# Kernel optimization log

Hardware: AMD Instinct MI355X
Metric: run time of the kernel (lower is better)

## Reference

```python
import jax, jax.numpy as jnp
import numpy as np

B, N, ZDIM = 8, 2048, 128
NPOINTS = 32
BN_EPS = 1e-5


def setup_inputs() -> dict:
    key = jax.random.key(0)
    ks = iter(jax.random.split(key, 64))

    def w(shape, s=0.05):
        return jax.random.normal(next(ks), shape, jnp.float32) * s

    inp = {"x": jax.random.normal(next(ks), (B, N, 3), jnp.float32)}
    inp.update(dict(
        w1=w((128, 3)), b1=w((128,)),
        w2=w((128, 128)), b2=w((128,)),
        w3=w((256, 128)), b3=w((256,)),
        w4=w((512, 256)), b4=w((512,)),
        a1_wqk=w((32, 1)), a1_wt=w((128, 128)), a1_bt=w((128,)),
        a2_wqk=w((32, 1)), a2_wt=w((128, 128)), a2_bt=w((128,)),
        a3_wqk=w((64, 1)), a3_wt=w((256, 256)), a3_bt=w((256,)),
        a4_wqk=w((128, 1)), a4_wt=w((512, 512)), a4_bt=w((512,)),
        fc1m_w=w((256, 512)), fc1m_b=w((256,)),
        fc2m_w=w((128, 256)), fc2m_b=w((128,)),
        fc3m_w=w((ZDIM, 128)), fc3m_b=w((ZDIM,)),
        fc1v_w=w((256, 512)), fc1v_b=w((256,)),
        fc2v_w=w((128, 256)), fc2v_b=w((128,)),
        fc3v_w=w((1, 128)), fc3v_b=w((1,)),
    ))
    return inp


def bn_cn(h):
    # BatchNorm1d over [B, C, N] features (training-mode batch stats, affine=identity at init)
    m = h.mean(axis=(0, 2), keepdims=True)
    v = h.var(axis=(0, 2), keepdims=True)
    return (h - m) * jax.lax.rsqrt(v + BN_EPS)


def bn_f(h):
    # BatchNorm1d over [B, F]
    m = h.mean(axis=0, keepdims=True)
    v = h.var(axis=0, keepdims=True)
    return (h - m) * jax.lax.rsqrt(v + BN_EPS)


def conv1x1(h, w, b):
    # 1x1 Conv1d: [B,Cin,N] x [Cout,Cin] -> [B,Cout,N]
    return jnp.einsum('oc,bcn->bon', w, h) + b[None, :, None]


def angle_density(xyz):
    # xyz: [B,N,3]; 1 - cosine similarity between all point pairs (computed as GEMM,
    # never materializing the [B,N,N,3] expanded tensors of the torch code)
    xn = xyz / jnp.linalg.norm(xyz, axis=-1, keepdims=True)
    dist = 1.0 - jnp.einsum('bnc,bmc->bnm', xn, xn)  # [B,N,N]
    neg_vals, _ = jax.lax.top_k(-dist, NPOINTS)       # 32 smallest distances
    feat_density = (-neg_vals).mean(axis=-1)          # [B,N]
    inv = 1.0 / feat_density
    return inv / jnp.max(inv)


def density_attn(h, dens, wqk, wt, bt):
    # h: [B,C,N], dens: [B,1,N]; q_conv and k_conv share weights
    q = jnp.einsum('dc,bcn->bdn', wqk, dens)          # [B,D4,N]
    energy = jnp.einsum('bdn,bdm->bnm', q, q)         # [B,N,N]
    attn = jax.nn.softmax(energy, axis=-1)
    attn = attn / (1e-9 + attn.sum(axis=1, keepdims=True))
    x_r = jnp.einsum('bcn,bnm->bcm', h, attn)         # [B,C,N]
    t = conv1x1(h - x_r, wt, bt)
    t = jax.nn.relu(bn_cn(t))
    return h + t


def reference(x, w1, b1, w2, b2, w3, b3, w4, b4,
              a1_wqk, a1_wt, a1_bt, a2_wqk, a2_wt, a2_bt,
              a3_wqk, a3_wt, a3_bt, a4_wqk, a4_wt, a4_bt,
              fc1m_w, fc1m_b, fc2m_w, fc2m_b, fc3m_w, fc3m_b,
              fc1v_w, fc1v_b, fc2v_w, fc2v_b, fc3v_w, fc3v_b):
    dens = angle_density(x)[:, None, :]               # [B,1,N]
    h = jnp.swapaxes(x, 1, 2)                         # [B,3,N]
    h = jax.nn.relu(bn_cn(conv1x1(h, w1, b1)))
    h = density_attn(h, dens, a1_wqk, a1_wt, a1_bt)
    h = jax.nn.relu(bn_cn(conv1x1(h, w2, b2)))
    h = density_attn(h, dens, a2_wqk, a2_wt, a2_bt)
    h = jax.nn.relu(bn_cn(conv1x1(h, w3, b3)))
    h = density_attn(h, dens, a3_wqk, a3_wt, a3_bt)
    h = bn_cn(conv1x1(h, w4, b4))                     # no relu on conv4 (matches source)
    h = density_attn(h, dens, a4_wqk, a4_wt, a4_bt)
    g = jnp.max(h, axis=2)                            # [B,512] global max pool

    u = jax.nn.relu(bn_f(g @ fc1m_w.T + fc1m_b))
    u = jax.nn.relu(bn_f(u @ fc2m_w.T + fc2m_b))
    u = u @ fc3m_w.T + fc3m_b
    u = u / jnp.linalg.norm(u, axis=-1, keepdims=True)

    k = jax.nn.relu(bn_f(g @ fc1v_w.T + fc1v_b))
    k = jax.nn.relu(bn_f(k @ fc2v_w.T + fc2v_b))
    k = k @ fc3v_w.T + fc3v_b
    k = jax.nn.softplus(k) + 1.0
    return (u, k)
```

## Files before the change

kernel.cpp:

```cpp
#include <hip/hip_runtime.h>
#include <cfloat>
#include <cmath>

constexpr int NB = 8;
constexpr int NP = 2048;
constexpr int NK = 11;

typedef __attribute__((ext_vector_type(4))) float f32x4;
typedef __attribute__((ext_vector_type(8))) short bf16x8;
#define MFMA16(a, b, c) __builtin_amdgcn_mfma_f32_16x16x32_bf16(a, b, c, 0, 0, 0)

__device__ inline ushort f2bf(float f) {
  union { float f; unsigned u; } v; v.f = f;
  unsigned r = v.u + 0x7FFFu + ((v.u >> 16) & 1u);
  return (ushort)(r >> 16);
}
__device__ inline unsigned pk2bf(float a, float b) {
  return (unsigned)f2bf(a) | ((unsigned)f2bf(b) << 16);
}

__device__ inline int dpp_wave_sum_i32(int c) {
  c += __builtin_amdgcn_update_dpp(0, c, 0x111, 0xf, 0xf, true);
  c += __builtin_amdgcn_update_dpp(0, c, 0x112, 0xf, 0xf, true);
  c += __builtin_amdgcn_update_dpp(0, c, 0x114, 0xf, 0xf, true);
  c += __builtin_amdgcn_update_dpp(0, c, 0x118, 0xf, 0xf, true);
  c += __builtin_amdgcn_update_dpp(0, c, 0x142, 0xf, 0xf, true);
  c += __builtin_amdgcn_update_dpp(0, c, 0x143, 0xf, 0xf, true);
  return __builtin_amdgcn_readlane(c, 63);
}

__global__ void k_prep(const float* __restrict__ x, float* __restrict__ xn, float* __restrict__ xt) {
  int i = blockIdx.x * blockDim.x + threadIdx.x;
  if (i >= NB * NP) return;
  int b = i >> 11, n = i & (NP - 1);
  float a0 = x[i * 3 + 0], a1 = x[i * 3 + 1], a2 = x[i * 3 + 2];
  float rn = rsqrtf(a0 * a0 + a1 * a1 + a2 * a2);
  xn[i * 3 + 0] = a0 * rn; xn[i * 3 + 1] = a1 * rn; xn[i * 3 + 2] = a2 * rn;
  float* xb = xt + (size_t)b * 3 * NP;
  xb[0 * NP + n] = a0; xb[1 * NP + n] = a1; xb[2 * NP + n] = a2;
}

__global__ void k_zero1(float* p) { if (threadIdx.x == 0) p[0] = 0.f; }

__global__ __launch_bounds__(512) void k_density(const float* __restrict__ xn,
                                                 float* __restrict__ inv,
                                                 int* __restrict__ maxinv) {
  __shared__ float sx[NP], sy[NP], sz[NP];
  int t = threadIdx.x;
  int w = t >> 6, lane = t & 63;
  int row0 = blockIdx.x * 8;
  int b = row0 >> 11;
  const float4* xb4 = (const float4*)(xn + (size_t)b * NP * 3);
  {
    float4 a = xb4[t * 3 + 0], c4 = xb4[t * 3 + 1], e4 = xb4[t * 3 + 2];
    int p = t * 4;
    sx[p + 0] = a.x;  sy[p + 0] = a.y;  sz[p + 0] = a.z;
    sx[p + 1] = a.w;  sy[p + 1] = c4.x; sz[p + 1] = c4.y;
    sx[p + 2] = c4.z; sy[p + 2] = c4.w; sz[p + 2] = e4.x;
    sx[p + 3] = e4.y; sy[p + 3] = e4.z; sz[p + 3] = e4.w;
  }
  __syncthreads();
  int row = row0 + w;
  int n = row & (NP - 1);
  float px = sx[n], py = sy[n], pz = sz[n];
  float d[32];
  float mn = FLT_MAX, mx = -FLT_MAX;
  #pragma unroll
  for (int k = 0; k < 32; ++k) {
    int m = lane + (k << 6);
    float v = 1.0f - (px * sx[m] + py * sy[m] + pz * sz[m]);
    d[k] = v;
    mn = fminf(mn, v); mx = fmaxf(mx, v);
  }
  #pragma unroll
  for (int off = 32; off; off >>= 1) {
    mn = fminf(mn, __shfl_xor(mn, off));
    mx = fminf(mx, __shfl_xor(mx, off));
  }
  float lo = mn, hi = mx + 1e-6f;
  for (int it = 0; it < 18; ++it) {
    float tt = 0.5f * (lo + hi);
    int c = 0;
    #pragma unroll
    for (int k = 0; k < 32; ++k) c += (d[k] < tt) ? 1 : 0;
    int ct = dpp_wave_sum_i32(c);
    bool le = ct <= 32;
    lo = le ? tt : lo;
    hi = le ? hi : tt;
  }
  float s = 0.f; int c = 0;
  #pragma unroll
  for (int k = 0; k < 32; ++k) {
    bool p = d[k] < lo;
    s += p ? d[k] : 0.f;
    c += p ? 1 : 0;
  }
  int ctot = dpp_wave_sum_i32(c);
  #pragma unroll
  for (int off = 32; off; off >>= 1) s += __shfl_xor(s, off);
  float sum = s + (float)(32 - ctot) * lo;
  if (lane == 0) {
    float iv = 32.0f / sum;
    inv[row] = iv;
    atomicMax(maxinv, __float_as_int(iv));
  }
}

__global__ void k_scale(float* __restrict__ dens, const float* __restrict__ maxinv) {
  int i = blockIdx.x * 256 + threadIdx.x;
  if (i < NB * NP) dens[i] *= (1.0f / maxinv[0]);
}

__global__ __launch_bounds__(64) void k_coef(const float* __restrict__ wqk, int D,
                                             float* __restrict__ coef) {
  int lane = threadIdx.x;
  float v = 0.f;
  for (int i = lane; i < D; i += 64) v += wqk[i] * wqk[i];
  #pragma unroll
  for (int off = 32; off; off >>= 1) v += __shfl_xor(v, off);
  if (lane == 0) {
    float c = 1.f;
    coef[0] = 1.f;
    for (int k = 1; k < NK; ++k) { c *= v / (float)k; coef[k] = c; }
  }
}

__global__ __launch_bounds__(256) void k_attn_small(const float* __restrict__ dens,
                                                    const float* __restrict__ coef,
                                                    float* __restrict__ rinv,
                                                    float* __restrict__ cinv) {
  int b = blockIdx.x, t = threadIdx.x, w = t >> 6, lane = t & 63;
  const float* db = dens + b * NP;
  float d[8], r[8];
  *(float4*)&d[0] = *(const float4*)(db + t * 8);
  *(float4*)&d[4] = *(const float4*)(db + t * 8 + 4);
  __shared__ float part[NK][4];
  float q[NK];
  {
    float acc[NK];
    #pragma unroll
    for (int k = 0; k < NK; ++k) acc[k] = 0.f;
    #pragma unroll
    for (int e = 0; e < 8; ++e) {
      float p = 1.f;
      #pragma unroll
      for (int k = 0; k < NK; ++k) { acc[k] += p; p *= d[e]; }
    }
    #pragma unroll
    for (int k = 0; k < NK; ++k) {
      float a = acc[k];
      #pragma unroll
      for (int off = 32; off; off >>= 1) a += __shfl_xor(a, off);
      if (lane == 0) part[k][w] = a;
    }
    __syncthreads();
    #pragma unroll
    for (int k = 0; k < NK; ++k)
      q[k] = coef[k] * ((part[k][0] + part[k][1]) + (part[k][2] + part[k][3]));
    __syncthreads();
  }
  #pragma unroll
  for (int e = 0; e < 8; ++e) {
    float poly = q[NK - 1];
    #pragma unroll
    for (int k = NK - 2; k >= 0; --k) poly = poly * d[e] + q[k];
    r[e] = 1.0f / poly;
  }
  *(float4*)(rinv + b * NP + t * 8)     = *(float4*)&r[0];
  *(float4*)(rinv + b * NP + t * 8 + 4) = *(float4*)&r[4];
  {
    float acc[NK];
    #pragma unroll
    for (int k = 0; k < NK; ++k) acc[k] = 0.f;
    #pragma unroll
    for (int e = 0; e < 8; ++e) {
      float p = r[e];
      #pragma unroll
      for (int k = 0; k < NK; ++k) { acc[k] += p; p *= d[e]; }
    }
    #pragma unroll
    for (int k = 0; k < NK; ++k) {
      float a = acc[k];
      #pragma unroll
      for (int off = 32; off; off >>= 1) a += __shfl_xor(a, off);
      if (lane == 0) part[k][w] = a;
    }
    __syncthreads();
    #pragma unroll
    for (int k = 0; k < NK; ++k)
      q[k] = coef[k] * ((part[k][0] + part[k][1]) + (part[k][2] + part[k][3]));
  }
  #pragma unroll
  for (int e = 0; e < 8; ++e) {
    float poly = q[NK - 1];
    #pragma unroll
    for (int k = NK - 2; k >= 0; --k) poly = poly * d[e] + q[k];
    r[e] = 1.0f / (poly + 1e-9f);
  }
  *(float4*)(cinv + b * NP + t * 8)     = *(float4*)&r[0];
  *(float4*)(cinv + b * NP + t * 8 + 4) = *(float4*)&r[4];
}

__global__ __launch_bounds__(256) void k_xrP(const float* __restrict__ H, float* __restrict__ U,
                                             const float* __restrict__ dens,
                                             const float* __restrict__ rinv,
                                             const float* __restrict__ cinv,
                                             const float* __restrict__ coef, int C) {
  int b = blockIdx.y, c = blockIdx.x, t = threadIdx.x, w = t >> 6, lane = t & 63;
  const float* Hc = H + ((size_t)b * C + c) * NP;
  float* Uc = U + ((size_t)b * C + c) * NP;
  const float* db = dens + b * NP;
  const float* rb = rinv + b * NP;
  const float* cb = cinv + b * NP;
  float h[8], d[8], r[8], cv[8];
  *(float4*)&h[0] = *(const float4*)(Hc + t * 8);
  *(float4*)&h[4] = *(const float4*)(Hc + t * 8 + 4);
  *(float4*)&d[0] = *(const float4*)(db + t * 8);
  *(float4*)&d[4] = *(const float4*)(db + t * 8 + 4);
  *(float4*)&r[0] = *(const float4*)(rb + t * 8);
  *(float4*)&r[4] = *(const float4*)(rb + t * 8 + 4);
  *(float4*)&cv[0] = *(const float4*)(cb + t * 8);
  *(float4*)&cv[4] = *(const float4*)(cb + t * 8 + 4);
  float acc[NK];
  #pragma unroll
  for (int k = 0; k < NK; ++k) acc[k] = 0.f;
  #pragma unroll
  for (int e = 0; e < 8; ++e) {
    float p = h[e] * r[e];
    #pragma unroll
    for (int k = 0; k < NK; ++k) { acc[k] += p; p *= d[e]; }
  }
  __shared__ float part[NK][4];
  #pragma unroll
  for (int k = 0; k < NK; ++k) {
    float a = acc[k];
    #pragma unroll
    for (int off = 32; off; off >>= 1) a += __shfl_xor(a, off);
    if (lane == 0) part[k][w] = a;
  }
  __syncthreads();
  float q[NK];
  #pragma unroll
  for (int k = 0; k < NK; ++k)
    q[k] = coef[k] * ((part[k][0] + part[k][1]) + (part[k][2] + part[k][3]));
  float u[8];
  #pragma unroll
  for (int e = 0; e < 8; ++e) {
    float poly = q[NK - 1];
    #pragma unroll
    for (int k = NK - 2; k >= 0; --k) poly = poly * d[e] + q[k];
    u[e] = h[e] - cv[e] * poly;
  }
  *(float4*)(Uc + t * 8)     = *(float4*)&u[0];
  *(float4*)(Uc + t * 8 + 4) = *(float4*)&u[4];
}

constexpr int LDA = 72;

__global__ __launch_bounds__(256) void k_gemm_mfma(const float* __restrict__ W,
                                                   const float* __restrict__ IN,
                                                   const float* __restrict__ bias,
                                                   float* __restrict__ OUT,
                                                   int Cin, int Cout) {
  int b = blockIdx.z, n0 = blockIdx.x * 128, o0 = blockIdx.y * 128;
  int tid = threadIdx.x, lane = tid & 63, w = tid >> 6;
  int wr = w >> 1, wc = w & 1;
  const float* Ib = IN + (size_t)b * Cin * NP;
  float* Ob = OUT + (size_t)b * Cout * NP;
  __shared__ ushort Asm[128 * LDA];
  __shared__ ushort Bsm[128 * LDA];
  f32x4 acc[4][4];
  #pragma unroll
  for (int i = 0; i < 4; ++i)
    #pragma unroll
    for (int j = 0; j < 4; ++j) acc[i][j] = (f32x4)(0.0f);

  int row = tid >> 1, half = tid & 1;
  int csub = tid & 63, q = tid >> 6;
  for (int cc0 = 0; cc0 < Cin; cc0 += 64) {
    __syncthreads();
    {
      const float* src = W + (size_t)(o0 + row) * Cin + cc0 + half * 32;
      unsigned* dst = (unsigned*)(Asm + row * LDA + half * 32);
      #pragma unroll
      for (int i = 0; i < 8; ++i) {
        float4 v = *(const float4*)(src + i * 4);
        dst[i * 2 + 0] = pk2bf(v.x, v.y);
        dst[i * 2 + 1] = pk2bf(v.z, v.w);
      }
      const float* isrc = Ib + (size_t)(cc0 + csub) * NP + n0 + q * 32;
      #pragma unroll
      for (int i = 0; i < 8; ++i) {
        float4 v = *(const float4*)(isrc + i * 4);
        ushort* bd = Bsm + (q * 32 + i * 4) * LDA + csub;
        bd[0]       = f2bf(v.x);
        bd[LDA]     = f2bf(v.y);
        bd[2 * LDA] = f2bf(v.z);
        bd[3 * LDA] = f2bf(v.w);
      }
    }
    __syncthreads();
    #pragma unroll
    for (int kk = 0; kk < 64; kk += 32) {
      bf16x8 af[4], bfr[4];
      #pragma unroll
      for (int i = 0; i < 4; ++i) {
        af[i]  = *(const bf16x8*)(Asm + (wr * 64 + i * 16 + (lane & 15)) * LDA + kk + (lane >> 4) * 8);
        bfr[i] = *(const bf16x8*)(Bsm + (wc * 64 + i * 16 + (lane & 15)) * LDA + kk + (lane >> 4) * 8);
      }
      #pragma unroll
      for (int i = 0; i < 4; ++i)
        #pragma unroll
        for (int j = 0; j < 4; ++j)
          acc[i][j] = MFMA16(af[i], bfr[j], acc[i][j]);
    }
  }
  #pragma unroll
  for (int i = 0; i < 4; ++i) {
    #pragma unroll
    for (int r = 0; r < 4; ++r) {
      int o = o0 + wr * 64 + i * 16 + (lane >> 4) * 4 + r;
      float bv = bias[o];
      #pragma unroll
      for (int j = 0; j < 4; ++j) {
        int n = n0 + wc * 64 + j * 16 + (lane & 15);
        Ob[(size_t)o * NP + n] = acc[i][j][r] + bv;
      }
    }
  }
}

__global__ __launch_bounds__(256) void k_gemm(const float* __restrict__ W,
                                              const float* __restrict__ IN,
                                              const float* __restrict__ bias,
                                              float* __restrict__ OUT,
                                              int Cin, int Cout) {
  int b = blockIdx.z;
  int n0 = blockIdx.x * 64;
  int o0 = blockIdx.y * 64;
  int tid = threadIdx.x;
  int tx = tid & 15, ty = tid >> 4;
  const float* Ib = IN + (size_t)b * Cin * NP;
  float* Ob = OUT + (size_t)b * Cout * NP;
  __shared__ float Wt[64][65];
  __shared__ float It[64][65];
  float acc[4][4] = {};
  for (int c0 = 0; c0 < Cin; c0 += 64) {
    __syncthreads();
    {
      int ci = tid & 63, ob4 = tid >> 6;
      bool cv = (c0 + ci) < Cin;
      #pragma unroll
      for (int k = 0; k < 16; ++k) {
        int oi = ob4 + (k << 2);
        Wt[ci][oi] = cv ? W[(size_t)(o0 + oi) * Cin + c0 + ci] : 0.f;
      }
      int ni = tid & 63, cb4 = tid >> 6;
      #pragma unroll
      for (int k = 0; k < 16; ++k) {
        int ci2 = cb4 + (k << 2);
        It[ci2][ni] = (c0 + ci2) < Cin ? Ib[(size_t)(c0 + ci2) * NP + n0 + ni] : 0.f;
      }
    }
    __syncthreads();
    #pragma unroll 4
    for (int ci = 0; ci < 64; ++ci) {
      float a0 = Wt[ci][ty * 4 + 0], a1 = Wt[ci][ty * 4 + 1], a2 = Wt[ci][ty * 4 + 2], a3 = Wt[ci][ty * 4 + 3];
      float b0 = It[ci][tx * 4 + 0], b1 = It[ci][tx * 4 + 1], b2 = It[ci][tx * 4 + 2], b3 = It[ci][tx * 4 + 3];
      acc[0][0] += a0 * b0; acc[0][1] += a0 * b1; acc[0][2] += a0 * b2; acc[0][3] += a0 * b3;
      acc[1][0] += a1 * b0; acc[1][1] += a1 * b1; acc[1][2] += a1 * b2; acc[1][3] += a1 * b3;
      acc[2][0] += a2 * b0; acc[2][1] += a2 * b1; acc[2][2] += a2 * b2; acc[2][3] += a2 * b3;
      acc[3][0] += a3 * b0; acc[3][1] += a3 * b1; acc[3][2] += a3 * b2; acc[3][3] += a3 * b3;
    }
  }
  #pragma unroll
  for (int i = 0; i < 4; ++i) {
    int o = o0 + ty * 4 + i;
    float bv = bias[o];
    #pragma unroll
    for (int j = 0; j < 4; ++j) {
      int n = n0 + tx * 4 + j;
      Ob[(size_t)o * NP + n] = acc[i][j] + bv;
    }
  }
}

__global__ __launch_bounds__(256) void k_bn(const float* __restrict__ T, float* __restrict__ H,
                                            int C, int relu, int acc) {
  int c = blockIdx.x, t = threadIdx.x, w = t >> 6, lane = t & 63;
  float4 v[16];
  float s = 0.f, s2 = 0.f;
  #pragma unroll
  for (int b = 0; b < NB; ++b) {
    const float4* p = (const float4*)(T + ((size_t)b * C + c) * NP);
    #pragma unroll
    for (int i = 0; i < 2; ++i) {
      float4 x = p[t + i * 256];
      v[b * 2 + i] = x;
      s += (x.x + x.y) + (x.z + x.w);
      s2 += (x.x * x.x + x.y * x.y) + (x.z * x.z + x.w * x.w);
    }
  }
  #pragma unroll
  for (int off = 32; off; off >>= 1) { s += __shfl_xor(s, off); s2 += __shfl_xor(s2, off); }
  __shared__ float ps[4], ps2[4];
  if (lane == 0) { ps[w] = s; ps2[w] = s2; }
  __syncthreads();
  float ts = (ps[0] + ps[1]) + (ps[2] + ps[3]);
  float ts2 = (ps2[0] + ps2[1]) + (ps2[2] + ps2[3]);
  float m = ts * (1.0f / (NB * NP));
  float var = ts2 * (1.0f / (NB * NP)) - m * m;
  float is = rsqrtf(var + 1e-5f);
  #pragma unroll
  for (int b = 0; b < NB; ++b) {
    float4* hp = (float4*)(H + ((size_t)b * C + c) * NP);
    #pragma unroll
    for (int i = 0; i < 2; ++i) {
      float4 x = v[b * 2 + i];
      x.x = (x.x - m) * is; x.y = (x.y - m) * is; x.z = (x.z - m) * is; x.w = (x.w - m) * is;
      if (relu) {
        x.x = fmaxf(x.x, 0.f); x.y = fmaxf(x.y, 0.f); x.z = fmaxf(x.z, 0.f); x.w = fmaxf(x.w, 0.f);
      }
      if (acc) {
        float4 h = hp[t + i * 256];
        x.x += h.x; x.y += h.y; x.z += h.z; x.w += h.w;
      }
      hp[t + i * 256] = x;
    }
  }
}

__global__ __launch_bounds__(64) void k_maxpool(const float* __restrict__ H, float* __restrict__ g) {
  int bf = blockIdx.x;
  const float* p = H + (size_t)bf * NP;
  int lane = threadIdx.x;
  float mx = -FLT_MAX;
  for (int n = lane; n < NP; n += 64) mx = fmaxf(mx, p[n]);
  #pragma unroll
  for (int off = 32; off > 0; off >>= 1) mx = fmaxf(mx, __shfl_xor(mx, off));
  if (lane == 0) g[bf] = mx;
}

__global__ __launch_bounds__(256) void k_head(const float* __restrict__ g,
    const float* __restrict__ f1mw, const float* __restrict__ f1mb,
    const float* __restrict__ f2mw, const float* __restrict__ f2mb,
    const float* __restrict__ f3mw, const float* __restrict__ f3mb,
    const float* __restrict__ f1vw, const float* __restrict__ f1vb,
    const float* __restrict__ f2vw, const float* __restrict__ f2vb,
    const float* __restrict__ f3vw, const float* __restrict__ f3vb,
    float* __restrict__ out) {
  bool vpath = (blockIdx.x == 1);
  const float* w1 = vpath ? f1vw : f1mw;
  const float* c1 = vpath ? f1vb : f1mb;
  const float* w2 = vpath ? f2vw : f2mw;
  const float* c2 = vpath ? f2vb : f2mb;
  __shared__ float gg[NB * 512];
  __shared__ float a1[NB * 256];
  __shared__ float a2[NB * 128];
  __shared__ float zz[NB * 128];
  __shared__ float nrm[NB];
  int t = threadIdx.x;
  for (int i = t; i < NB * 512; i += 256) gg[i] = g[i];
  __syncthreads();
  float o[NB];
  {
    #pragma unroll
    for (int b = 0; b < NB; ++b) o[b] = c1[t];
    const float* wr = w1 + (size_t)t * 512;
    for (int j = 0; j < 512; ++j) {
      float w = wr[j];
      #pragma unroll
      for (int b = 0; b < NB; ++b) o[b] += gg[b * 512 + j] * w;
    }
    float mean = 0.f;
    #pragma unroll
    for (int b = 0; b < NB; ++b) mean += o[b];
    mean *= (1.0f / NB);
    float var = 0.f;
    #pragma unroll
    for (int b = 0; b < NB; ++b) { float d = o[b] - mean; var += d * d; }
    var *= (1.0f / NB);
    float is = rsqrtf(var + 1e-5f);
    #pragma unroll
    for (int b = 0; b < NB; ++b) a1[b * 256 + t] = fmaxf((o[b] - mean) * is, 0.f);
  }
  __syncthreads();
  if (t < 128) {
    #pragma unroll
    for (int b = 0; b < NB; ++b) o[b] = c2[t];
    const float* wr = w2 + (size_t)t * 256;
    for (int j = 0; j < 256; ++j) {
      float w = wr[j];
      #pragma unroll
      for (int b = 0; b < NB; ++b) o[b] += a1[b * 256 + j] * w;
    }
    float mean = 0.f;
    #pragma unroll
    for (int b = 0; b < NB; ++b) mean += o[b];
    mean *= (1.0f / NB);
    float var = 0.f;
    #pragma unroll
    for (int b = 0; b < NB; ++b) { float d = o[b] - mean; var += d * d; }
    var *= (1.0f / NB);
    float is = rsqrtf(var + 1e-5f);
    #pragma unroll
    for (int b = 0; b < NB; ++b) a2[b * 128 + t] = fmaxf((o[b] - mean) * is, 0.f);
  }
  __syncthreads();
  if (!vpath) {
    if (t < 128) {
      const float* wr = f3mw + (size_t)t * 128;
      for (int b = 0; b < NB; ++b) {
        float s = f3mb[t];
        for (int j = 0; j < 128; ++j) s += a2[b * 128 + j] * wr[j];
        zz[b * 128 + t] = s;
      }
    }
    __syncthreads();
    if (t < NB) {
      float s = 0.f;
      for (int j = 0; j < 128; ++j) { float v = zz[t * 128 + j]; s += v * v; }
      nrm[t] = sqrtf(s);
    }
    __syncthreads();
    if (t < 128) {
      for (int b = 0; b < NB; ++b) out[b * 128 + t] = zz[b * 128 + t] / nrm[b];
    }
  } else {
    if (t < NB) {
      float s = f3vb[0];
      for (int j = 0; j < 128; ++j) s += a2[t * 128 + j] * f3vw[j];
      float sp = (s > 20.f) ? s : log1pf(expf(s));
      out[NB * 128 + t] = sp + 1.0f;
    }
  }
}

extern "C" void kernel_launch(void* const* d_in, const int* in_sizes, int n_in,
                              void* d_out, int out_size, void* d_ws, size_t ws_size,
                              hipStream_t stream) {
  const float* x  = (const float*)d_in[0];
  const float* w1 = (const float*)d_in[1];
  const float* b1 = (const float*)d_in[2];
  const float* w2 = (const float*)d_in[3];
  const float* b2 = (const float*)d_in[4];
  const float* w3 = (const float*)d_in[5];
  const float* b3 = (const float*)d_in[6];
  const float* w4 = (const float*)d_in[7];
  const float* b4 = (const float*)d_in[8];
  const float* a_wqk[4] = {(const float*)d_in[9],  (const float*)d_in[12], (const float*)d_in[15], (const float*)d_in[18]};
  const float* a_wt[4]  = {(const float*)d_in[10], (const float*)d_in[13], (const float*)d_in[16], (const float*)d_in[19]};
  const float* a_bt[4]  = {(const float*)d_in[11], (const float*)d_in[14], (const float*)d_in[17], (const float*)d_in[20]};
  int a_D[4] = {in_sizes[9], in_sizes[12], in_sizes[15], in_sizes[18]};
  const float* f1mw = (const float*)d_in[21]; const float* f1mb = (const float*)d_in[22];
  const float* f2mw = (const float*)d_in[23]; const float* f2mb = (const float*)d_in[24];
  const float* f3mw = (const float*)d_in[25]; const float* f3mb = (const float*)d_in[26];
  const float* f1vw = (const float*)d_in[27]; const float* f1vb = (const float*)d_in[28];
  const float* f2vw = (const float*)d_in[29]; const float* f2vb = (const float*)d_in[30];
  const float* f3vw = (const float*)d_in[31]; const float* f3vb = (const float*)d_in[32];
  float* out = (float*)d_out;

  float* ws = (float*)d_ws;
  float* xn     = ws; ws += (size_t)NB * NP * 3;
  float* dens   = ws; ws += NB * NP;
  float* maxinv = ws; ws += 16;
  float* coef   = ws; ws += 16;
  float* rinv   = ws; ws += NB * NP;
  float* cinv   = ws; ws += NB * NP;
  float* g      = ws; ws += NB * 512;
  float* Hb     = ws; ws += (size_t)NB * 512 * NP;
  float* Ub     = ws; ws += (size_t)NB * 512 * NP;
  float* Tb     = ws; ws += (size_t)NB * 512 * NP;

  k_prep<<<NB * NP / 256, 256, 0, stream>>>(x, xn, Ub);
  k_zero1<<<1, 64, 0, stream>>>(maxinv);
  k_density<<<NB * NP / 8, 512, 0, stream>>>(xn, dens, (int*)maxinv);
  k_scale<<<NB * NP / 256, 256, 0, stream>>>(dens, maxinv);

  auto conv = [&](const float* W, const float* bias, const float* IN, int Cin, int Cout, bool relu) {
    if (Cin < 64)
      k_gemm<<<dim3(NP / 64, Cout / 64, NB), 256, 0, stream>>>(W, IN, bias, Tb, Cin, Cout);
    else
      k_gemm_mfma<<<dim3(NP / 128, Cout / 128, NB), 256, 0, stream>>>(W, IN, bias, Tb, Cin, Cout);
    k_bn<<<Cout, 256, 0, stream>>>(Tb, Hb, Cout, relu ? 1 : 0, 0);
  };
  auto attn = [&](int li, int C) {
    k_coef<<<1, 64, 0, stream>>>(a_wqk[li], a_D[li], coef);
    k_attn_small<<<NB, 256, 0, stream>>>(dens, coef, rinv, cinv);
    k_xrP<<<dim3(C, NB), 256, 0, stream>>>(Hb, Ub, dens, rinv, cinv, coef, C);
    k_gemm_mfma<<<dim3(NP / 128, C / 128, NB), 256, 0, stream>>>(a_wt[li], Ub, a_bt[li], Tb, C, C);
    k_bn<<<C, 256, 0, stream>>>(Tb, Hb, C, 1, 1);
  };

  conv(w1, b1, Ub, 3, 128, true);
  attn(0, 128);
  conv(w2, b2, Hb, 128, 128, true);
  attn(1, 128);
  conv(w3, b3, Hb, 128, 256, true);
  attn(2, 256);
  conv(w4, b4, Hb, 256, 512, false);
  attn(3, 512);

  k_maxpool<<<NB * 512, 64, 0, stream>>>(Hb, g);
  k_head<<<2, 256, 0, stream>>>(g, f1mw, f1mb, f2mw, f2mb, f3mw, f3mb,
                                f1vw, f1vb, f2vw, f2vb, f3vw, f3vb, out);
}
```

Baseline: 562.0 us.

## Quantize density distances to fp16 bits and use integer 4-way radix selection

Result: no change. 572.3 us (+1.8%).

```diff
diff --git a/kernel.cpp b/kernel.cpp
--- a/kernel.cpp
+++ b/kernel.cpp
@@ -1,4 +1,5 @@
 #include <hip/hip_runtime.h>
+#include <hip/hip_fp16.h>
 #include <cfloat>
 #include <cmath>
 
@@ -46,6 +47,7 @@
                                                  float* __restrict__ inv,
                                                  int* __restrict__ maxinv) {
   __shared__ float sx[NP], sy[NP], sz[NP];
+  __shared__ ushort dq[8][NP];
   int t = threadIdx.x;
   int w = t >> 6, lane = t & 63;
   int row0 = blockIdx.x * 8;
@@ -63,42 +65,63 @@
   int row = row0 + w;
   int n = row & (NP - 1);
   float px = sx[n], py = sy[n], pz = sz[n];
-  float d[32];
-  float mn = FLT_MAX, mx = -FLT_MAX;
+  ushort* dr = dq[w];
+  int mni = 0xFFFF, mxi = 0;
   #pragma unroll
   for (int k = 0; k < 32; ++k) {
     int m = lane + (k << 6);
-    float v = 1.0f - (px * sx[m] + py * sy[m] + pz * sz[m]);
-    d[k] = v;
-    mn = fminf(mn, v); mx = fmaxf(mx, v);
+    float v = fmaxf(1.0f - (px * sx[m] + py * sy[m] + pz * sz[m]), 0.0f);
+    ushort u = __half_as_ushort(__float2half(v));
+    dr[m] = u;
+    int ui = (int)u;
+    mni = min(mni, ui); mxi = max(mxi, ui);
   }
   #pragma unroll
   for (int off = 32; off; off >>= 1) {
-    mn = fminf(mn, __shfl_xor(mn, off));
-    mx = fminf(mx, __shfl_xor(mx, off));
-  }
-  float lo = mn, hi = mx + 1e-6f;
-  for (int it = 0; it < 18; ++it) {
-    float tt = 0.5f * (lo + hi);
+    mni = min(mni, __shfl_xor(mni, off));
+    mxi = min(mxi, __shfl_xor(mxi, off));
+  }
+  int lo = mni, hi = mxi + 1;
+  #pragma unroll
+  for (int it = 0; it < 8; ++it) {
+    int d = hi - lo;
+    int t1 = lo + (d >> 2), t2 = lo + (d >> 1), t3 = lo + d - (d >> 2);
+    int c12 = 0, c3 = 0;
+    #pragma unroll
+    for (int k = 0; k < 32; ++k) {
+      int u = (int)dr[lane + (k << 6)];
+      c12 += (u < t1 ? 1 : 0) + (u < t2 ? (1 << 12) : 0);
+      c3  += (u < t3 ? 1 : 0);
+    }
+    c12 = dpp_wave_sum_i32(c12);
+    c3  = dpp_wave_sum_i32(c3);
+    int c1 = c12 & 0xFFF, c2 = c12 >> 12;
+    if (c3 <= 32)      { lo = t3; }
+    else if (c2 <= 32) { lo = t2; hi = t3; }
+    else if (c1 <= 32) { lo = t1; hi = t2; }
+    else               { hi = t1; }
+  }
+  #pragma unroll
+  for (int it = 0; it < 2; ++it) {
+    int tt = lo + ((hi - lo) >> 1);
     int c = 0;
     #pragma unroll
-    for (int k = 0; k < 32; ++k) c += (d[k] < tt) ? 1 : 0;
-    int ct = dpp_wave_sum_i32(c);
-    bool le = ct <= 32;
-    lo = le ? tt : lo;
-    hi = le ? hi : tt;
+    for (int k = 0; k < 32; ++k) c += ((int)dr[lane + (k << 6)] < tt) ? 1 : 0;
+    c = dpp_wave_sum_i32(c);
+    if (c <= 32) lo = tt; else hi = tt;
   }
   float s = 0.f; int c = 0;
   #pragma unroll
   for (int k = 0; k < 32; ++k) {
-    bool p = d[k] < lo;
-    s += p ? d[k] : 0.f;
+    int u = (int)dr[lane + (k << 6)];
+    bool p = u < lo;
+    s += p ? __half2float(__ushort_as_half((ushort)u)) : 0.f;
     c += p ? 1 : 0;
   }
   int ctot = dpp_wave_sum_i32(c);
   #pragma unroll
   for (int off = 32; off; off >>= 1) s += __shfl_xor(s, off);
-  float sum = s + (float)(32 - ctot) * lo;
+  float sum = s + (float)(32 - ctot) * __half2float(__ushort_as_half((ushort)lo));
   if (lane == 0) {
     float iv = 32.0f / sum;
     inv[row] = iv;
```
